# Optimization experiments

Hardware: AMD Instinct MI355X
Metric: run time of the kernel (lower is better)

Reference implementation:

```python
import jax, jax.numpy as jnp
import numpy as np

MANT_BITS = 8  # static quantize_param_dict values for Positional_0/1/2
_PWL_X = jnp.linspace(-4.0, 4.0, 33, dtype=jnp.float32)
_PWL_Y = 0.5 * _PWL_X * (1.0 + jax.lax.erf(_PWL_X / jnp.sqrt(jnp.float32(2.0))))


def float2fix(x, mantissa_bits):
    """Fixed-point quantization: round to multiples of 2^-mantissa_bits (STE grad)."""
    s = jnp.float32(2.0 ** mantissa_bits)
    q = jnp.round(x * s) / s
    return x + jax.lax.stop_gradient(q - x)


def pwlin_gelu_basic(x, mantissa_bits_in, mantissa_bits_out):
    """Piecewise-linear GELU: quantized input, linear interp of exact GELU on
    [-4,4] (33 breakpoints), 0 for x<-4, identity for x>4, quantized output."""
    xq = float2fix(x, mantissa_bits_in)
    y = jnp.interp(xq, _PWL_X, _PWL_Y)
    y = jnp.where(xq > 4.0, xq, jnp.where(xq < -4.0, jnp.float32(0.0), y))
    return float2fix(y, mantissa_bits_out)


def setup_inputs() -> dict:
    key = jax.random.key(0)
    k_x, k_w1, k_b1, k_w2, k_b2 = jax.random.split(key, 5)
    dim, ff_dim = 1024, 4096
    B, S = 32, 512
    sc1 = 1.0 / np.sqrt(dim)
    sc2 = 1.0 / np.sqrt(ff_dim)
    return {
        "x": jax.random.normal(k_x, (B, S, dim), dtype=jnp.float32),
        "w1": jax.random.uniform(k_w1, (dim, ff_dim), jnp.float32, -sc1, sc1),
        "b1": jax.random.uniform(k_b1, (ff_dim,), jnp.float32, -sc1, sc1),
        "w2": jax.random.uniform(k_w2, (ff_dim, dim), jnp.float32, -sc2, sc2),
        "b2": jax.random.uniform(k_b2, (dim,), jnp.float32, -sc2, sc2),
    }


def reference(x, w1, b1, w2, b2):
    # fc1 GEMM + quantize epilogue
    h = jnp.einsum("bsd,df->bsf", x, w1) + b1          # [B,S,ff_dim]
    h = float2fix(h, MANT_BITS)                         # Positional_0
    # piecewise-linear GELU with quantized in/out
    h = pwlin_gelu_basic(h, MANT_BITS, MANT_BITS)
    h = float2fix(h, MANT_BITS)                         # Positional_1
    # fc2 GEMM + quantize epilogue
    out = jnp.einsum("bsf,fd->bsd", h, w2) + b2         # [B,S,dim]
    return float2fix(out, MANT_BITS)                    # Positional_2
```

## Files before the change

kernel.cpp:

```cpp
#include <hip/hip_runtime.h>
#include <hip/hip_bf16.h>

typedef __bf16 bf16_t;
typedef __bf16 bf16x8 __attribute__((ext_vector_type(8)));
typedef __bf16 bf16x4 __attribute__((ext_vector_type(4)));
typedef float f32x4 __attribute__((ext_vector_type(4)));

#define QS   256.0f
#define QINV 0.00390625f

__device__ __forceinline__ void async_copy16(const bf16_t* g, bf16_t* l) {
  __builtin_amdgcn_global_load_lds(
      (__attribute__((address_space(1))) void*)g,
      (__attribute__((address_space(3))) void*)l,
      16, 0, 0);
}

template <int SHIFT>
__device__ __forceinline__ void stage_unit(const bf16_t* __restrict__ gk, bf16_t* lbuf,
                                           int K, int halfOff, int tid) {
  const int scb = (((tid & 7) ^ ((tid >> 3) & 7)) << 3);
  const int MASK = (1 << SHIFT) - 1;
#pragma unroll
  for (int q = 0; q < 2; ++q) {
    const int u  = q * 64 + (tid >> 3);
    const int u0 = q * 64 + ((tid >> 6) << 3);
    const int row  = halfOff + (u  & MASK) + ((u  >> SHIFT) << (SHIFT + 1));
    const int row0 = halfOff + (u0 & MASK) + ((u0 >> SHIFT) << (SHIFT + 1));
    async_copy16(gk + (size_t)row * K + scb, lbuf + row0 * 64);
  }
}

__device__ __forceinline__ bf16x8 ldfrag(const bf16_t* buf, int row, int ks, int lq) {
  const int phys = ((ks << 2) | lq) ^ (row & 7);
  return *(const bf16x8*)(buf + row * 64 + (phys << 3));
}

__device__ __forceinline__ void ktile(
    const bf16_t* __restrict__ Ab, const bf16_t* __restrict__ Bb,
    bf16_t* __restrict__ An, bf16_t* __restrict__ Bn,
    const bf16_t* __restrict__ aN, const bf16_t* __restrict__ bN,
    const bool nl, const int tid, const int rA0, const int rB0, const int lq,
    const int K, f32x4 (&acc)[8][4]) {
  bf16x8 fa[2][4];
  bf16x8 fb[2][2][2];

#pragma unroll
  for (int ks = 0; ks < 2; ++ks) {
#pragma unroll
    for (int i = 0; i < 4; ++i) fa[ks][i] = ldfrag(Ab, rA0 + i * 16, ks, lq);
#pragma unroll
    for (int j = 0; j < 2; ++j) fb[0][ks][j] = ldfrag(Bb, rB0 + j * 16, ks, lq);
  }
  if (nl) {
    stage_unit<6>(aN, An, K, 0, tid);
    asm volatile("s_waitcnt vmcnt(4)" ::: "memory");
  } else {
    asm volatile("s_waitcnt vmcnt(2)" ::: "memory");
  }
  __builtin_amdgcn_s_barrier();
  asm volatile("s_waitcnt lgkmcnt(0)" ::: "memory");
  __builtin_amdgcn_sched_barrier(0);
  __builtin_amdgcn_s_setprio(1);
#pragma unroll
  for (int ks = 0; ks < 2; ++ks)
#pragma unroll
    for (int i = 0; i < 4; ++i)
#pragma unroll
      for (int j = 0; j < 2; ++j)
        acc[i][j] = __builtin_amdgcn_mfma_f32_16x16x32_bf16(fa[ks][i], fb[0][ks][j], acc[i][j], 0, 0, 0);
  __builtin_amdgcn_s_setprio(0);
  __builtin_amdgcn_s_barrier();

#pragma unroll
  for (int ks = 0; ks < 2; ++ks)
#pragma unroll
    for (int j = 0; j < 2; ++j) fb[1][ks][j] = ldfrag(Bb, rB0 + 32 + j * 16, ks, lq);
  if (nl) {
    stage_unit<5>(bN, Bn, K, 0, tid);
    asm volatile("s_waitcnt vmcnt(4)" ::: "memory");
  } else {
    asm volatile("s_waitcnt vmcnt(0)" ::: "memory");
  }
  __builtin_amdgcn_s_barrier();
  asm volatile("s_waitcnt lgkmcnt(0)" ::: "memory");
  __builtin_amdgcn_sched_barrier(0);
  __builtin_amdgcn_s_setprio(1);
#pragma unroll
  for (int ks = 0; ks < 2; ++ks)
#pragma unroll
    for (int i = 0; i < 4; ++i)
#pragma unroll
      for (int j = 0; j < 2; ++j)
        acc[i][2 + j] = __builtin_amdgcn_mfma_f32_16x16x32_bf16(fa[ks][i], fb[1][ks][j], acc[i][2 + j], 0, 0, 0);
  __builtin_amdgcn_s_setprio(0);
  __builtin_amdgcn_s_barrier();

#pragma unroll
  for (int ks = 0; ks < 2; ++ks)
#pragma unroll
    for (int i = 0; i < 4; ++i) fa[ks][i] = ldfrag(Ab, rA0 + 64 + i * 16, ks, lq);
  if (nl) stage_unit<5>(bN, Bn, K, 32, tid);
  __builtin_amdgcn_s_barrier();
  asm volatile("s_waitcnt lgkmcnt(0)" ::: "memory");
  __builtin_amdgcn_sched_barrier(0);
  __builtin_amdgcn_s_setprio(1);
#pragma unroll
  for (int ks = 0; ks < 2; ++ks)
#pragma unroll
    for (int i = 0; i < 4; ++i)
#pragma unroll
      for (int j = 0; j < 2; ++j)
        acc[4 + i][2 + j] = __builtin_amdgcn_mfma_f32_16x16x32_bf16(fa[ks][i], fb[1][ks][j], acc[4 + i][2 + j], 0, 0, 0);
  __builtin_amdgcn_s_setprio(0);
  __builtin_amdgcn_s_barrier();

  if (nl) {
    stage_unit<6>(aN, An, K, 64, tid);
    asm volatile("s_waitcnt vmcnt(4)" ::: "memory");
  }
  __builtin_amdgcn_s_barrier();
  __builtin_amdgcn_sched_barrier(0);
  __builtin_amdgcn_s_setprio(1);
#pragma unroll
  for (int ks = 0; ks < 2; ++ks)
#pragma unroll
    for (int i = 0; i < 4; ++i)
#pragma unroll
      for (int j = 0; j < 2; ++j)
        acc[4 + i][j] = __builtin_amdgcn_mfma_f32_16x16x32_bf16(fa[ks][i], fb[0][ks][j], acc[4 + i][j], 0, 0, 0);
  __builtin_amdgcn_s_setprio(0);
  __builtin_amdgcn_s_barrier();
}

template <bool GELU, typename OutT, bool XSWZ>
__global__ __launch_bounds__(512, 2)
void gemm_tile(const bf16_t* __restrict__ A, const bf16_t* __restrict__ Bt,
               const float* __restrict__ bias, OutT* __restrict__ C,
               int M, int N, int K) {
  __shared__ __attribute__((aligned(16))) bf16_t As0[256 * 64];
  __shared__ __attribute__((aligned(16))) bf16_t Bs0[256 * 64];
  __shared__ __attribute__((aligned(16))) bf16_t As1[256 * 64];
  __shared__ __attribute__((aligned(16))) bf16_t Bs1[256 * 64];

  const int tid = threadIdx.x;
  const int lane = tid & 63;
  const int wid = tid >> 6;
  const int wr = wid >> 2;
  const int wc = wid & 3;
  const int l15 = lane & 15;
  const int lq = lane >> 4;

  float ytA = 0.f, ytS = 0.f;
  if (GELU) {
    float xv = -4.0f + 0.25f * (float)lane;
    float y0 = 0.5f * xv * (1.0f + erff(xv * 0.70710678f));
    float xv1 = xv + 0.25f;
    float y1 = 0.5f * xv1 * (1.0f + erff(xv1 * 0.70710678f));
    ytA = y0;
    ytS = y1 - y0;
  }

  int bx = blockIdx.x, by = blockIdx.y;
  if (XSWZ) {
    const int gx = gridDim.x;
    const int nwg = gx * gridDim.y;
    const int f = by * gx + bx;
    const int chunk = nwg >> 3;
    const int f2 = (f & 7) * chunk + (f >> 3);
    bx = f2 % gx;
    by = f2 / gx;
  }

  const int mBase = by * 256;
  const int nBase = bx * 256;
  const bf16_t* aTile = A + (size_t)mBase * K;
  const bf16_t* bTile = Bt + (size_t)nBase * K;

  f32x4 acc[8][4];
#pragma unroll
  for (int i = 0; i < 8; ++i)
#pragma unroll
    for (int j = 0; j < 4; ++j)
      acc[i][j] = (f32x4){0.f, 0.f, 0.f, 0.f};

  const int nT = K >> 6;
  const int rA0 = wr * 128 + l15;
  const int rB0 = wc * 64 + l15;

  stage_unit<6>(aTile, As0, K, 0, tid);
  stage_unit<5>(bTile, Bs0, K, 0, tid);
  stage_unit<5>(bTile, Bs0, K, 32, tid);
  stage_unit<6>(aTile, As0, K, 64, tid);
  asm volatile("s_waitcnt vmcnt(4)" ::: "memory");
  __builtin_amdgcn_s_barrier();

  for (int tt = 0; tt < nT; tt += 2) {
    ktile(As0, Bs0, As1, Bs1,
          aTile + (size_t)(tt + 1) * 64, bTile + (size_t)(tt + 1) * 64,
          true, tid, rA0, rB0, lq, K, acc);
    ktile(As1, Bs1, As0, Bs0,
          aTile + (size_t)(tt + 2) * 64, bTile + (size_t)(tt + 2) * 64,
          (tt + 2 < nT), tid, rA0, rB0, lq, K, acc);
  }

  float bj[4];
#pragma unroll
  for (int j = 0; j < 4; ++j)
    bj[j] = bias[nBase + wc * 64 + j * 16 + l15];

#pragma unroll
  for (int i = 0; i < 8; ++i) {
    const int rb = mBase + wr * 128 + i * 16 + lq * 4;
#pragma unroll
    for (int j = 0; j < 4; ++j) {
      const int cn = nBase + wc * 64 + j * 16 + l15;
#pragma unroll
      for (int r = 0; r < 4; ++r) {
        float c = acc[i][j][r] + bj[j];
        float v;
        if (GELU) {
          float xq = rintf(c * QS) * QINV;
          float t = (xq + 4.0f) * 4.0f;
          int ii = (int)t;
          ii = ii < 0 ? 0 : (ii > 31 ? 31 : ii);
          float f = t - (float)ii;
          float y0 = __shfl(ytA, ii);
          float sl = __shfl(ytS, ii);
          v = fmaf(f, sl, y0);
          v = (xq > 4.0f) ? xq : v;
          v = (xq < -4.0f) ? 0.0f : v;
          v = rintf(v * QS) * QINV;
        } else {
          v = rintf(c * QS) * QINV;
        }
        C[(size_t)(rb + r) * N + cn] = (OutT)v;
      }
    }
  }
}

__global__ void cvt_bf16_kernel(const float* __restrict__ in, bf16_t* __restrict__ out, int n4) {
  int idx = blockIdx.x * blockDim.x + threadIdx.x;
  if (idx < n4) {
    const float4 v = ((const float4*)in)[idx];
    bf16x4 o;
    o[0] = (bf16_t)v.x; o[1] = (bf16_t)v.y; o[2] = (bf16_t)v.z; o[3] = (bf16_t)v.w;
    ((bf16x4*)out)[idx] = o;
  }
}

__global__ void transpose_cvt_kernel(const float* __restrict__ in, bf16_t* __restrict__ out,
                                     int R, int C) {
  __shared__ float t[32][33];
  const int c0 = blockIdx.x * 32;
  const int r0 = blockIdx.y * 32;
  const int tx = threadIdx.x;
  const int ty = threadIdx.y;
#pragma unroll
  for (int dy = 0; dy < 32; dy += 8)
    t[ty + dy][tx] = in[(size_t)(r0 + ty + dy) * C + c0 + tx];
  __syncthreads();
#pragma unroll
  for (int dy = 0; dy < 32; dy += 8)
    out[(size_t)(c0 + ty + dy) * R + r0 + tx] = (bf16_t)t[tx][ty + dy];
}

extern "C" void kernel_launch(void* const* d_in, const int* in_sizes, int n_in,
                              void* d_out, int out_size, void* d_ws, size_t ws_size,
                              hipStream_t stream) {
  const float* x  = (const float*)d_in[0];
  const float* w1 = (const float*)d_in[1];
  const float* b1 = (const float*)d_in[2];
  const float* w2 = (const float*)d_in[3];
  const float* b2 = (const float*)d_in[4];
  float* out = (float*)d_out;

  const int M = 16384, D = 1024, F = 4096;

  char* ws = (char*)d_ws;
  size_t off = 0;
  bf16_t* xb  = (bf16_t*)(ws + off); off += (size_t)M * D * 2;
  bf16_t* w1t = (bf16_t*)(ws + off); off += (size_t)D * F * 2;
  bf16_t* w2t = (bf16_t*)(ws + off); off += (size_t)F * D * 2;
  bf16_t* h   = (bf16_t*)(ws + off);

  cvt_bf16_kernel<<<(M * D / 4 + 255) / 256, 256, 0, stream>>>(x, xb, M * D / 4);
  transpose_cvt_kernel<<<dim3(F / 32, D / 32), dim3(32, 8), 0, stream>>>(w1, w1t, D, F);
  transpose_cvt_kernel<<<dim3(D / 32, F / 32), dim3(32, 8), 0, stream>>>(w2, w2t, F, D);

  gemm_tile<true, bf16_t, false><<<dim3(F / 256, M / 256), 512, 0, stream>>>(xb, w1t, b1, h, M, F, D);
  gemm_tile<false, float, true><<<dim3(D / 256, M / 256), 512, 0, stream>>>(h, w2t, b2, out, M, D, F);
}
```

Before: 417.1 us.

## Prefetch two K-tiles ahead in GEMM and merge prep kernels into one launch

The GEMM main loop now loads the tile two steps ahead into the buffer being consumed, instead of one step ahead into the alternate buffer. The prologue preloads both LDS buffers, and the vmcnt waits are reworked to match the deeper queue. This is meant to hide more global-load latency behind MFMA work. Separately, the three conversion and transpose kernels are merged into one launch to cut launch overhead, at the cost of more complex wait-count bookkeeping.

Measured after the change: 424.3 us. About the same (+1.7%).

```diff
diff --git a/kernel.cpp b/kernel.cpp
--- a/kernel.cpp
+++ b/kernel.cpp
@@ -38,9 +38,10 @@
 
 __device__ __forceinline__ void ktile(
     const bf16_t* __restrict__ Ab, const bf16_t* __restrict__ Bb,
-    bf16_t* __restrict__ An, bf16_t* __restrict__ Bn,
-    const bf16_t* __restrict__ aN, const bf16_t* __restrict__ bN,
-    const bool nl, const int tid, const int rA0, const int rB0, const int lq,
+    bf16_t* __restrict__ Aw, bf16_t* __restrict__ Bw,
+    const bf16_t* __restrict__ aN2, const bf16_t* __restrict__ bN2,
+    const bool stage2, const int wsel0, const int wsel3,
+    const int tid, const int rA0, const int rB0, const int lq,
     const int K, f32x4 (&acc)[8][4]) {
   bf16x8 fa[2][4];
   bf16x8 fb[2][2][2];
@@ -52,12 +53,8 @@
 #pragma unroll
     for (int j = 0; j < 2; ++j) fb[0][ks][j] = ldfrag(Bb, rB0 + j * 16, ks, lq);
   }
-  if (nl) {
-    stage_unit<6>(aN, An, K, 0, tid);
-    asm volatile("s_waitcnt vmcnt(4)" ::: "memory");
-  } else {
-    asm volatile("s_waitcnt vmcnt(2)" ::: "memory");
-  }
+  if (wsel0 == 0) { asm volatile("s_waitcnt vmcnt(8)" ::: "memory"); }
+  else            { asm volatile("s_waitcnt vmcnt(0)" ::: "memory"); }
   __builtin_amdgcn_s_barrier();
   asm volatile("s_waitcnt lgkmcnt(0)" ::: "memory");
   __builtin_amdgcn_sched_barrier(0);
@@ -76,12 +73,6 @@
   for (int ks = 0; ks < 2; ++ks)
 #pragma unroll
     for (int j = 0; j < 2; ++j) fb[1][ks][j] = ldfrag(Bb, rB0 + 32 + j * 16, ks, lq);
-  if (nl) {
-    stage_unit<5>(bN, Bn, K, 0, tid);
-    asm volatile("s_waitcnt vmcnt(4)" ::: "memory");
-  } else {
-    asm volatile("s_waitcnt vmcnt(0)" ::: "memory");
-  }
   __builtin_amdgcn_s_barrier();
   asm volatile("s_waitcnt lgkmcnt(0)" ::: "memory");
   __builtin_amdgcn_sched_barrier(0);
@@ -100,7 +91,10 @@
   for (int ks = 0; ks < 2; ++ks)
 #pragma unroll
     for (int i = 0; i < 4; ++i) fa[ks][i] = ldfrag(Ab, rA0 + 64 + i * 16, ks, lq);
-  if (nl) stage_unit<5>(bN, Bn, K, 32, tid);
+  if (stage2) {
+    stage_unit<6>(aN2, Aw, K, 0, tid);
+    stage_unit<5>(bN2, Bw, K, 0, tid);
+  }
   __builtin_amdgcn_s_barrier();
   asm volatile("s_waitcnt lgkmcnt(0)" ::: "memory");
   __builtin_amdgcn_sched_barrier(0);
@@ -115,10 +109,12 @@
   __builtin_amdgcn_s_setprio(0);
   __builtin_amdgcn_s_barrier();
 
-  if (nl) {
-    stage_unit<6>(aN, An, K, 64, tid);
-    asm volatile("s_waitcnt vmcnt(4)" ::: "memory");
-  }
+  if (stage2) {
+    stage_unit<5>(bN2, Bw, K, 32, tid);
+    stage_unit<6>(aN2, Aw, K, 64, tid);
+  }
+  if (wsel3 == 0)      { asm volatile("s_waitcnt vmcnt(12)" ::: "memory"); }
+  else if (wsel3 == 1) { asm volatile("s_waitcnt vmcnt(4)"  ::: "memory"); }
   __builtin_amdgcn_s_barrier();
   __builtin_amdgcn_sched_barrier(0);
   __builtin_amdgcn_s_setprio(1);
@@ -192,16 +188,23 @@
   stage_unit<5>(bTile, Bs0, K, 0, tid);
   stage_unit<5>(bTile, Bs0, K, 32, tid);
   stage_unit<6>(aTile, As0, K, 64, tid);
-  asm volatile("s_waitcnt vmcnt(4)" ::: "memory");
+  stage_unit<6>(aTile + 64, As1, K, 0, tid);
+  stage_unit<5>(bTile + 64, Bs1, K, 0, tid);
+  stage_unit<5>(bTile + 64, Bs1, K, 32, tid);
+  stage_unit<6>(aTile + 64, As1, K, 64, tid);
+  asm volatile("s_waitcnt vmcnt(12)" ::: "memory");
   __builtin_amdgcn_s_barrier();
 
   for (int tt = 0; tt < nT; tt += 2) {
-    ktile(As0, Bs0, As1, Bs1,
-          aTile + (size_t)(tt + 1) * 64, bTile + (size_t)(tt + 1) * 64,
-          true, tid, rA0, rB0, lq, K, acc);
-    ktile(As1, Bs1, As0, Bs0,
+    ktile(As0, Bs0, As0, Bs0,
           aTile + (size_t)(tt + 2) * 64, bTile + (size_t)(tt + 2) * 64,
-          (tt + 2 < nT), tid, rA0, rB0, lq, K, acc);
+          tt + 2 < nT, 0, (tt + 2 < nT) ? 0 : 1,
+          tid, rA0, rB0, lq, K, acc);
+    ktile(As1, Bs1, As1, Bs1,
+          aTile + (size_t)(tt + 3) * 64, bTile + (size_t)(tt + 3) * 64,
+          tt + 3 < nT, (tt + 1 == nT - 1) ? 1 : 0,
+          (tt + 3 < nT) ? 0 : ((tt + 2 < nT) ? 1 : 2),
+          tid, rA0, rB0, lq, K, acc);
   }
 
   float bj[4];
@@ -240,30 +243,42 @@
   }
 }
 
-__global__ void cvt_bf16_kernel(const float* __restrict__ in, bf16_t* __restrict__ out, int n4) {
-  int idx = blockIdx.x * blockDim.x + threadIdx.x;
-  if (idx < n4) {
-    const float4 v = ((const float4*)in)[idx];
+__global__ __launch_bounds__(256)
+void prep_kernel(const float* __restrict__ x, bf16_t* __restrict__ xb,
+                 const float* __restrict__ w1, bf16_t* __restrict__ w1t,
+                 const float* __restrict__ w2, bf16_t* __restrict__ w2t) {
+  __shared__ float t[32][33];
+  const int id = blockIdx.x;
+  const int tid = threadIdx.x;
+  if (id < 16384) {
+    const int idx = id * 256 + tid;
+    const float4 v = ((const float4*)x)[idx];
     bf16x4 o;
     o[0] = (bf16_t)v.x; o[1] = (bf16_t)v.y; o[2] = (bf16_t)v.z; o[3] = (bf16_t)v.w;
-    ((bf16x4*)out)[idx] = o;
-  }
-}
-
-__global__ void transpose_cvt_kernel(const float* __restrict__ in, bf16_t* __restrict__ out,
-                                     int R, int C) {
-  __shared__ float t[32][33];
-  const int c0 = blockIdx.x * 32;
-  const int r0 = blockIdx.y * 32;
-  const int tx = threadIdx.x;
-  const int ty = threadIdx.y;
-#pragma unroll
-  for (int dy = 0; dy < 32; dy += 8)
-    t[ty + dy][tx] = in[(size_t)(r0 + ty + dy) * C + c0 + tx];
-  __syncthreads();
-#pragma unroll
-  for (int dy = 0; dy < 32; dy += 8)
-    out[(size_t)(c0 + ty + dy) * R + r0 + tx] = (bf16_t)t[tx][ty + dy];
+    ((bf16x4*)xb)[idx] = o;
+  } else {
+    const float* in; bf16_t* out; int R, C, bx, by;
+    if (id < 20480) {
+      const int id2 = id - 16384;
+      in = w1; out = w1t; R = 1024; C = 4096;
+      bx = id2 & 127; by = id2 >> 7;
+    } else {
+      const int id3 = id - 20480;
+      in = w2; out = w2t; R = 4096; C = 1024;
+      bx = id3 & 31; by = id3 >> 5;
+    }
+    const int c0 = bx * 32;
+    const int r0 = by * 32;
+    const int tx = tid & 31;
+    const int ty = tid >> 5;
+#pragma unroll
+    for (int dy = 0; dy < 32; dy += 8)
+      t[ty + dy][tx] = in[(size_t)(r0 + ty + dy) * C + c0 + tx];
+    __syncthreads();
+#pragma unroll
+    for (int dy = 0; dy < 32; dy += 8)
+      out[(size_t)(c0 + ty + dy) * R + r0 + tx] = (bf16_t)t[tx][ty + dy];
+  }
 }
 
 extern "C" void kernel_launch(void* const* d_in, const int* in_sizes, int n_in,
@@ -285,9 +300,7 @@
   bf16_t* w2t = (bf16_t*)(ws + off); off += (size_t)F * D * 2;
   bf16_t* h   = (bf16_t*)(ws + off);
 
-  cvt_bf16_kernel<<<(M * D / 4 + 255) / 256, 256, 0, stream>>>(x, xb, M * D / 4);
-  transpose_cvt_kernel<<<dim3(F / 32, D / 32), dim3(32, 8), 0, stream>>>(w1, w1t, D, F);
-  transpose_cvt_kernel<<<dim3(D / 32, F / 32), dim3(32, 8), 0, stream>>>(w2, w2t, F, D);
+  prep_kernel<<<16384 + 4096 + 4096, 256, 0, stream>>>(x, xb, w1, w1t, w2, w2t);
 
   gemm_tile<true, bf16_t, false><<<dim3(F / 256, M / 256), 512, 0, stream>>>(xb, w1t, b1, h, M, F, D);
   gemm_tile<false, float, true><<<dim3(D / 256, M / 256), 512, 0, stream>>>(h, w2t, b2, out, M, D, F);
```
